# Optimization experiments

Hardware: AMD Instinct MI355X
Metric: run time of the kernel (lower is better)

## Reference

```python
import jax, jax.numpy as jnp
import numpy as np

N, C, F = 64, 128, 2048


def setup_inputs() -> dict:
    key = jax.random.key(0)
    kx, ka = jax.random.split(key)
    X = jax.random.normal(kx, (N, C, F), dtype=jnp.float32)
    # Glorot-uniform init for A [C, C, F]: fan_in = C*F, fan_out = C*F
    limit = np.sqrt(6.0 / (C * F + C * F)).astype(np.float32)
    A = jax.random.uniform(ka, (C, C, F), dtype=jnp.float32, minval=-limit, maxval=limit)
    return {"X": X, "A": A}


def reference(X, A):
    # scores: reduce feature dim F -> [N, C, M]
    c = jnp.einsum('ncf,cmf->ncm', X, A)
    W = jax.nn.softmax(c, axis=-1)  # attention over source channels M
    # combine: mix channels of X with attention weights -> [N, C, F]
    return jnp.einsum('nmf,ncm->ncf', X, W)
```

## Files before the change

### kernel.cpp

```cpp
#include <hip/hip_runtime.h>
#include <hip/hip_bf16.h>


typedef __attribute__((ext_vector_type(8))) short bf16x8;
typedef __attribute__((ext_vector_type(4))) float f32x4;

#define PART_ELEMS (64 * 128 * 128)
#define WOFF_BYTES (4ull * PART_ELEMS * 4ull)

static __device__ __forceinline__ unsigned f2bf_pk(float a, float b) {
    unsigned ua = __float_as_uint(a);
    unsigned ub = __float_as_uint(b);
    ua = (ua + 0x7FFFu + ((ua >> 16) & 1u)) >> 16;
    ub = (ub + 0x7FFFu + ((ub >> 16) & 1u)) >> 16;
    return ua | (ub << 16);
}

__global__ __launch_bounds__(256, 2) void k_scores(const float* __restrict__ X,
                                                   const float* __restrict__ A,
                                                   float* __restrict__ part) {
    __shared__ short Xt[64 * 72];
    __shared__ short At[128 * 72];

    const int bx = blockIdx.x;
    const int c  = bx >> 2;
    const int p  = bx & 3;
    const int t  = threadIdx.x;
    const int l  = t & 63;
    const int w  = t >> 6;
    const int wn = (w & 1) * 32;
    const int wm = (w >> 1) * 64;
    const int l15 = l & 15;
    const int lg  = l >> 4;

    f32x4 acc[2][4];
#pragma unroll
    for (int i = 0; i < 2; ++i)
#pragma unroll
        for (int j = 0; j < 4; ++j) acc[i][j] = (f32x4)0.0f;

    const int fq    = (t & 15) * 4;
    const int rbase = t >> 4;

    const float* Xg = X + ((size_t)rbase * 128 + c) * 2048 + p * 512 + fq;
    const float* Ag = A + ((size_t)c * 128 + rbase) * 2048 + p * 512 + fq;

    for (int kb = 0; kb < 8; ++kb) {
        const int f0 = kb * 64;
#pragma unroll
        for (int j = 0; j < 4; ++j) {
            float4 v = *(const float4*)(Xg + (size_t)j * (16 * 128 * 2048) + f0);
            *(uint2*)&Xt[(rbase + 16 * j) * 72 + fq] =
                make_uint2(f2bf_pk(v.x, v.y), f2bf_pk(v.z, v.w));
        }
#pragma unroll
        for (int j = 0; j < 8; ++j) {
            float4 v = *(const float4*)(Ag + (size_t)j * (16 * 2048) + f0);
            *(uint2*)&At[(rbase + 16 * j) * 72 + fq] =
                make_uint2(f2bf_pk(v.x, v.y), f2bf_pk(v.z, v.w));
        }
        __syncthreads();
#pragma unroll
        for (int ks = 0; ks < 2; ++ks) {
            const int ko = ks * 32 + lg * 8;
            bf16x8 a[2], b[4];
#pragma unroll
            for (int i = 0; i < 2; ++i)
                a[i] = *(const bf16x8*)&Xt[(wn + 16 * i + l15) * 72 + ko];
#pragma unroll
            for (int j = 0; j < 4; ++j)
                b[j] = *(const bf16x8*)&At[(wm + 16 * j + l15) * 72 + ko];
#pragma unroll
            for (int i = 0; i < 2; ++i)
#pragma unroll
                for (int j = 0; j < 4; ++j)
                    acc[i][j] = __builtin_amdgcn_mfma_f32_16x16x32_bf16(a[i], b[j], acc[i][j], 0, 0, 0);
        }
        __syncthreads();
    }

    float* outp = part + (size_t)p * PART_ELEMS;
#pragma unroll
    for (int i = 0; i < 2; ++i) {
        const int nb = wn + 16 * i + lg * 4;
#pragma unroll
        for (int j = 0; j < 4; ++j) {
            const int m = wm + 16 * j + l15;
#pragma unroll
            for (int r = 0; r < 4; ++r)
                outp[(size_t)(nb + r) * 16384 + c * 128 + m] = acc[i][j][r];
        }
    }
}

__global__ __launch_bounds__(256) void k_softmax(const float* __restrict__ part,
                                                 unsigned int* __restrict__ Wout) {
    const int t   = threadIdx.x;
    const int l   = t & 63;
    const int row = blockIdx.x * 4 + (t >> 6);

    const float* s = part + (size_t)row * 128 + 2 * l;
    float v0 = 0.f, v1 = 0.f;
#pragma unroll
    for (int p = 0; p < 4; ++p) {
        float2 v = *(const float2*)(s + (size_t)p * PART_ELEMS);
        v0 += v.x; v1 += v.y;
    }
    float mx = fmaxf(v0, v1);
#pragma unroll
    for (int d = 1; d < 64; d <<= 1) mx = fmaxf(mx, __shfl_xor(mx, d, 64));
    float e0 = __expf(v0 - mx), e1 = __expf(v1 - mx);
    float sm = e0 + e1;
#pragma unroll
    for (int d = 1; d < 64; d <<= 1) sm += __shfl_xor(sm, d, 64);
    const float inv = 1.0f / sm;
    Wout[(size_t)row * 64 + l] = f2bf_pk(e0 * inv, e1 * inv);
}

__global__ __launch_bounds__(256, 2) void k_combine(const float* __restrict__ X,
                                                    const unsigned short* __restrict__ W,
                                                    float* __restrict__ out) {
    __shared__ short Wl[128 * 136];
    __shared__ short T[128 * 40];

    const int bx = blockIdx.x;
    const int n  = bx >> 4;
    const int f0 = (bx & 15) * 128;
    const int t  = threadIdx.x;
    const int l  = t & 63;
    const int w  = t >> 6;
    const int l15 = l & 15;
    const int lg  = l >> 4;
    const int wc = (w >> 1) * 64;
    const int wf = (w & 1) * 64;

    {
        const int c = t >> 1;
        const int h = (t & 1) * 64;
        const unsigned short* src = W + ((size_t)n * 128 + c) * 128 + h;
#pragma unroll
        for (int j = 0; j < 8; ++j) {
            bf16x8 v = *(const bf16x8*)(src + j * 8);
            *(bf16x8*)&Wl[c * 136 + h + j * 8] = v;
        }
    }

    f32x4 acc[4][4];
#pragma unroll
    for (int i = 0; i < 4; ++i)
#pragma unroll
        for (int j = 0; j < 4; ++j) acc[i][j] = (f32x4)0.0f;

    const int mpr = (t & 15) * 2;
    const int fqu = (t >> 4) * 4;

    for (int m0 = 0; m0 < 128; m0 += 32) {
        __syncthreads();
#pragma unroll
        for (int pass = 0; pass < 2; ++pass) {
            const int fl = fqu + 64 * pass;
            const float* g = X + ((size_t)n * 128 + m0 + mpr) * 2048 + f0 + fl;
            float4 x0 = *(const float4*)g;
            float4 x1 = *(const float4*)(g + 2048);
            unsigned* Tw = (unsigned*)T;
            Tw[(fl + 0) * 20 + (mpr >> 1)] = f2bf_pk(x0.x, x1.x);
            Tw[(fl + 1) * 20 + (mpr >> 1)] = f2bf_pk(x0.y, x1.y);
            Tw[(fl + 2) * 20 + (mpr >> 1)] = f2bf_pk(x0.z, x1.z);
            Tw[(fl + 3) * 20 + (mpr >> 1)] = f2bf_pk(x0.w, x1.w);
        }
        __syncthreads();
        const int ko = lg * 8;
        bf16x8 a[4], b[4];
#pragma unroll
        for (int i = 0; i < 4; ++i)
            a[i] = *(const bf16x8*)&Wl[(wc + 16 * i + l15) * 136 + m0 + ko];
#pragma unroll
        for (int j = 0; j < 4; ++j)
            b[j] = *(const bf16x8*)&T[(wf + 16 * j + l15) * 40 + ko];
#pragma unroll
        for (int i = 0; i < 4; ++i)
#pragma unroll
            for (int j = 0; j < 4; ++j)
                acc[i][j] = __builtin_amdgcn_mfma_f32_16x16x32_bf16(a[i], b[j], acc[i][j], 0, 0, 0);
    }

#pragma unroll
    for (int i = 0; i < 4; ++i) {
        const int c = wc + 16 * i + lg * 4;
#pragma unroll
        for (int j = 0; j < 4; ++j) {
            const int f = f0 + wf + 16 * j + l15;
            float* o = out + ((size_t)n * 128 + c) * 2048 + f;
#pragma unroll
            for (int r = 0; r < 4; ++r) o[(size_t)r * 2048] = acc[i][j][r];
        }
    }
}

extern "C" void kernel_launch(void* const* d_in, const int* in_sizes, int n_in,
                              void* d_out, int out_size, void* d_ws, size_t ws_size,
                              hipStream_t stream) {
    const float* X = (const float*)d_in[0];
    const float* A = (const float*)d_in[1];
    float* out = (float*)d_out;

    float* part = (float*)d_ws;
    unsigned short* W = (unsigned short*)((char*)d_ws + WOFF_BYTES);

    k_scores<<<dim3(512), dim3(256), 0, stream>>>(X, A, part);
    k_softmax<<<dim3(2048), dim3(256), 0, stream>>>(part, (unsigned int*)W);
    k_combine<<<dim3(1024), dim3(256), 0, stream>>>(X, W, out);
}
```

Baseline: 283.1 us.

## Use direct global-to-LDS loads, bf16 partials, and 8-way F split

Both GEMM kernels now load fp32 tiles straight into LDS with global_load_lds using XOR-swizzled layouts, and convert to bf16 at fragment-read time instead of through registers before the LDS store. The score kernel splits F into 8 parts instead of 4, doubling block count, and raises the occupancy hint. Partial scores are stored as bf16, halving partial traffic to softmax. The bf16 partial sums lose precision before softmax, and storing fp32 in LDS doubles its footprint per tile.

```diff
diff --git a/kernel.cpp b/kernel.cpp
--- a/kernel.cpp
+++ b/kernel.cpp
@@ -1,12 +1,11 @@
 #include <hip/hip_runtime.h>
-#include <hip/hip_bf16.h>
 
 
 typedef __attribute__((ext_vector_type(8))) short bf16x8;
 typedef __attribute__((ext_vector_type(4))) float f32x4;
 
-#define PART_ELEMS (64 * 128 * 128)
-#define WOFF_BYTES (4ull * PART_ELEMS * 4ull)
+#define PART_E (64 * 128 * 128)
+#define NP 8
 
 static __device__ __forceinline__ unsigned f2bf_pk(float a, float b) {
     unsigned ua = __float_as_uint(a);
@@ -15,23 +14,46 @@
     ub = (ub + 0x7FFFu + ((ub >> 16) & 1u)) >> 16;
     return ua | (ub << 16);
 }
-
-__global__ __launch_bounds__(256, 2) void k_scores(const float* __restrict__ X,
+static __device__ __forceinline__ unsigned short f2bf1(float a) {
+    unsigned ua = __float_as_uint(a);
+    ua = (ua + 0x7FFFu + ((ua >> 16) & 1u)) >> 16;
+    return (unsigned short)ua;
+}
+static __device__ __forceinline__ float bf2f(unsigned s) {
+    return __uint_as_float(s << 16);
+}
+static __device__ __forceinline__ void gl_lds16(const void* g, void* l) {
+    __builtin_amdgcn_global_load_lds((const __attribute__((address_space(1))) void*)g,
+                                     (__attribute__((address_space(3))) void*)l, 16, 0, 0);
+}
+static __device__ __forceinline__ bf16x8 cvt8(float4 lo, float4 hi) {
+    union { bf16x8 v; unsigned u[4]; } r;
+    r.u[0] = f2bf_pk(lo.x, lo.y);
+    r.u[1] = f2bf_pk(lo.z, lo.w);
+    r.u[2] = f2bf_pk(hi.x, hi.y);
+    r.u[3] = f2bf_pk(hi.z, hi.w);
+    return r.v;
+}
+
+__global__ __launch_bounds__(256, 4) void k_scores(const float* __restrict__ X,
                                                    const float* __restrict__ A,
-                                                   float* __restrict__ part) {
-    __shared__ short Xt[64 * 72];
-    __shared__ short At[128 * 72];
+                                                   unsigned short* __restrict__ part) {
+    __shared__ float Xs[64 * 32];
+    __shared__ float As[128 * 32];
 
     const int bx = blockIdx.x;
-    const int c  = bx >> 2;
-    const int p  = bx & 3;
-    const int t  = threadIdx.x;
-    const int l  = t & 63;
-    const int w  = t >> 6;
+    const int c = bx >> 3;
+    const int p = bx & 7;
+    const int t = threadIdx.x;
+    const int l = t & 63;
+    const int w = t >> 6;
+    const int l15 = l & 15;
+    const int lg = l >> 4;
     const int wn = (w & 1) * 32;
     const int wm = (w >> 1) * 64;
-    const int l15 = l & 15;
-    const int lg  = l >> 4;
+
+    const int lr = l >> 3;
+    const int lq = (l & 7) ^ lr;
 
     f32x4 acc[2][4];
 #pragma unroll
@@ -39,47 +61,45 @@
 #pragma unroll
         for (int j = 0; j < 4; ++j) acc[i][j] = (f32x4)0.0f;
 
-    const int fq    = (t & 15) * 4;
-    const int rbase = t >> 4;
-
-    const float* Xg = X + ((size_t)rbase * 128 + c) * 2048 + p * 512 + fq;
-    const float* Ag = A + ((size_t)c * 128 + rbase) * 2048 + p * 512 + fq;
+    const int s0 = (lg * 2) ^ (l15 & 7);
+    const int s1 = (lg * 2 + 1) ^ (l15 & 7);
 
     for (int kb = 0; kb < 8; ++kb) {
-        const int f0 = kb * 64;
-#pragma unroll
-        for (int j = 0; j < 4; ++j) {
-            float4 v = *(const float4*)(Xg + (size_t)j * (16 * 128 * 2048) + f0);
-            *(uint2*)&Xt[(rbase + 16 * j) * 72 + fq] =
-                make_uint2(f2bf_pk(v.x, v.y), f2bf_pk(v.z, v.w));
-        }
-#pragma unroll
-        for (int j = 0; j < 8; ++j) {
-            float4 v = *(const float4*)(Ag + (size_t)j * (16 * 2048) + f0);
-            *(uint2*)&At[(rbase + 16 * j) * 72 + fq] =
-                make_uint2(f2bf_pk(v.x, v.y), f2bf_pk(v.z, v.w));
-        }
-        __syncthreads();
-#pragma unroll
-        for (int ks = 0; ks < 2; ++ks) {
-            const int ko = ks * 32 + lg * 8;
-            bf16x8 a[2], b[4];
-#pragma unroll
-            for (int i = 0; i < 2; ++i)
-                a[i] = *(const bf16x8*)&Xt[(wn + 16 * i + l15) * 72 + ko];
+        const int f = p * 256 + kb * 32 + lq * 4;
+#pragma unroll
+        for (int ii = 0; ii < 2; ++ii) {
+            const int I = 2 * w + ii;
+            const int r = I * 8 + lr;
+            gl_lds16(X + ((size_t)r * 128 + c) * 2048 + f, &Xs[I * 256]);
+        }
+#pragma unroll
+        for (int ii = 0; ii < 4; ++ii) {
+            const int I = 4 * w + ii;
+            const int r = I * 8 + lr;
+            gl_lds16(A + ((size_t)c * 128 + r) * 2048 + f, &As[I * 256]);
+        }
+        __syncthreads();
+
+        bf16x8 a[2], b[4];
+#pragma unroll
+        for (int i = 0; i < 2; ++i) {
+            const float4* row = (const float4*)&Xs[(wn + 16 * i + l15) * 32];
+            a[i] = cvt8(row[s0], row[s1]);
+        }
+#pragma unroll
+        for (int j = 0; j < 4; ++j) {
+            const float4* row = (const float4*)&As[(wm + 16 * j + l15) * 32];
+            b[j] = cvt8(row[s0], row[s1]);
+        }
+#pragma unroll
+        for (int i = 0; i < 2; ++i)
 #pragma unroll
             for (int j = 0; j < 4; ++j)
-                b[j] = *(const bf16x8*)&At[(wm + 16 * j + l15) * 72 + ko];
-#pragma unroll
-            for (int i = 0; i < 2; ++i)
-#pragma unroll
-                for (int j = 0; j < 4; ++j)
-                    acc[i][j] = __builtin_amdgcn_mfma_f32_16x16x32_bf16(a[i], b[j], acc[i][j], 0, 0, 0);
-        }
-        __syncthreads();
-    }
-
-    float* outp = part + (size_t)p * PART_ELEMS;
+                acc[i][j] = __builtin_amdgcn_mfma_f32_16x16x32_bf16(a[i], b[j], acc[i][j], 0, 0, 0);
+        __syncthreads();
+    }
+
+    unsigned short* op = part + (size_t)p * PART_E;
 #pragma unroll
     for (int i = 0; i < 2; ++i) {
         const int nb = wn + 16 * i + lg * 4;
@@ -88,23 +108,23 @@
             const int m = wm + 16 * j + l15;
 #pragma unroll
             for (int r = 0; r < 4; ++r)
-                outp[(size_t)(nb + r) * 16384 + c * 128 + m] = acc[i][j][r];
-        }
-    }
-}
-
-__global__ __launch_bounds__(256) void k_softmax(const float* __restrict__ part,
+                op[((size_t)(nb + r) * 128 + c) * 128 + m] = f2bf1(acc[i][j][r]);
+        }
+    }
+}
+
+__global__ __launch_bounds__(256) void k_softmax(const unsigned int* __restrict__ part,
                                                  unsigned int* __restrict__ Wout) {
-    const int t   = threadIdx.x;
-    const int l   = t & 63;
+    const int t = threadIdx.x;
+    const int l = t & 63;
     const int row = blockIdx.x * 4 + (t >> 6);
 
-    const float* s = part + (size_t)row * 128 + 2 * l;
     float v0 = 0.f, v1 = 0.f;
 #pragma unroll
-    for (int p = 0; p < 4; ++p) {
-        float2 v = *(const float2*)(s + (size_t)p * PART_ELEMS);
-        v0 += v.x; v1 += v.y;
+    for (int p = 0; p < NP; ++p) {
+        unsigned u = part[(size_t)p * (PART_E / 2) + (size_t)row * 64 + l];
+        v0 += bf2f(u & 0xFFFFu);
+        v1 += bf2f(u >> 16);
     }
     float mx = fmaxf(v0, v1);
 #pragma unroll
@@ -117,31 +137,32 @@
     Wout[(size_t)row * 64 + l] = f2bf_pk(e0 * inv, e1 * inv);
 }
 
-__global__ __launch_bounds__(256, 2) void k_combine(const float* __restrict__ X,
+__global__ __launch_bounds__(256, 3) void k_combine(const float* __restrict__ X,
                                                     const unsigned short* __restrict__ W,
                                                     float* __restrict__ out) {
-    __shared__ short Wl[128 * 136];
-    __shared__ short T[128 * 40];
+    __shared__ unsigned short Wl[128 * 128];
+    __shared__ float Xs[32 * 128];
 
     const int bx = blockIdx.x;
-    const int n  = bx >> 4;
+    const int n = bx >> 4;
     const int f0 = (bx & 15) * 128;
-    const int t  = threadIdx.x;
-    const int l  = t & 63;
-    const int w  = t >> 6;
+    const int t = threadIdx.x;
+    const int l = t & 63;
+    const int w = t >> 6;
     const int l15 = l & 15;
-    const int lg  = l >> 4;
+    const int lg = l >> 4;
     const int wc = (w >> 1) * 64;
     const int wf = (w & 1) * 64;
 
     {
-        const int c = t >> 1;
-        const int h = (t & 1) * 64;
-        const unsigned short* src = W + ((size_t)n * 128 + c) * 128 + h;
-#pragma unroll
-        for (int j = 0; j < 8; ++j) {
-            bf16x8 v = *(const bf16x8*)(src + j * 8);
-            *(bf16x8*)&Wl[c * 136 + h + j * 8] = v;
+        const int lr = l >> 4;
+        const int sl = l & 15;
+#pragma unroll
+        for (int ii = 0; ii < 8; ++ii) {
+            const int I = 8 * w + ii;
+            const int r = I * 4 + lr;
+            const int q = (sl & 8) | ((sl ^ r) & 7);
+            gl_lds16(W + (size_t)n * 16384 + r * 128 + q * 8, &Wl[I * 512]);
         }
     }
 
@@ -151,37 +172,45 @@
 #pragma unroll
         for (int j = 0; j < 4; ++j) acc[i][j] = (f32x4)0.0f;
 
-    const int mpr = (t & 15) * 2;
-    const int fqu = (t >> 4) * 4;
+    const int lr2 = l >> 5;
+    const int q2 = l & 31;
 
     for (int m0 = 0; m0 < 128; m0 += 32) {
-        __syncthreads();
-#pragma unroll
-        for (int pass = 0; pass < 2; ++pass) {
-            const int fl = fqu + 64 * pass;
-            const float* g = X + ((size_t)n * 128 + m0 + mpr) * 2048 + f0 + fl;
-            float4 x0 = *(const float4*)g;
-            float4 x1 = *(const float4*)(g + 2048);
-            unsigned* Tw = (unsigned*)T;
-            Tw[(fl + 0) * 20 + (mpr >> 1)] = f2bf_pk(x0.x, x1.x);
-            Tw[(fl + 1) * 20 + (mpr >> 1)] = f2bf_pk(x0.y, x1.y);
-            Tw[(fl + 2) * 20 + (mpr >> 1)] = f2bf_pk(x0.z, x1.z);
-            Tw[(fl + 3) * 20 + (mpr >> 1)] = f2bf_pk(x0.w, x1.w);
-        }
-        __syncthreads();
-        const int ko = lg * 8;
+#pragma unroll
+        for (int ii = 0; ii < 4; ++ii) {
+            const int I = 4 * w + ii;
+            const int r = I * 2 + lr2;
+            gl_lds16(X + ((size_t)n * 128 + m0 + r) * 2048 + f0 + q2 * 4, &Xs[I * 256]);
+        }
+        __syncthreads();
+
         bf16x8 a[4], b[4];
 #pragma unroll
-        for (int i = 0; i < 4; ++i)
-            a[i] = *(const bf16x8*)&Wl[(wc + 16 * i + l15) * 136 + m0 + ko];
-#pragma unroll
-        for (int j = 0; j < 4; ++j)
-            b[j] = *(const bf16x8*)&T[(wf + 16 * j + l15) * 40 + ko];
+        for (int i = 0; i < 4; ++i) {
+            const int cr = wc + 16 * i + l15;
+            const int q = (m0 >> 3) + lg;
+            const int s = (q & 8) | ((q ^ cr) & 7);
+            a[i] = *(const bf16x8*)&Wl[cr * 128 + s * 8];
+        }
+#pragma unroll
+        for (int j = 0; j < 4; ++j) {
+            const float* col = &Xs[(lg * 8) * 128 + wf + 16 * j + l15];
+            float v[8];
+#pragma unroll
+            for (int rr = 0; rr < 8; ++rr) v[rr] = col[rr * 128];
+            union { bf16x8 bv; unsigned u[4]; } r_;
+            r_.u[0] = f2bf_pk(v[0], v[1]);
+            r_.u[1] = f2bf_pk(v[2], v[3]);
+            r_.u[2] = f2bf_pk(v[4], v[5]);
+            r_.u[3] = f2bf_pk(v[6], v[7]);
+            b[j] = r_.bv;
+        }
 #pragma unroll
         for (int i = 0; i < 4; ++i)
 #pragma unroll
             for (int j = 0; j < 4; ++j)
                 acc[i][j] = __builtin_amdgcn_mfma_f32_16x16x32_bf16(a[i], b[j], acc[i][j], 0, 0, 0);
+        __syncthreads();
     }
 
 #pragma unroll
@@ -204,10 +233,10 @@
     const float* A = (const float*)d_in[1];
     float* out = (float*)d_out;
 
-    float* part = (float*)d_ws;
-    unsigned short* W = (unsigned short*)((char*)d_ws + WOFF_BYTES);
-
-    k_scores<<<dim3(512), dim3(256), 0, stream>>>(X, A, part);
-    k_softmax<<<dim3(2048), dim3(256), 0, stream>>>(part, (unsigned int*)W);
-    k_combine<<<dim3(1024), dim3(256), 0, stream>>>(X, W, out);
-}
+    unsigned short* part = (unsigned short*)d_ws;
+    unsigned short* Wb = part + (size_t)NP * PART_E;
+
+    k_scores<<<dim3(1024), dim3(256), 0, stream>>>(X, A, part);
+    k_softmax<<<dim3(2048), dim3(256), 0, stream>>>((const unsigned int*)part, (unsigned int*)Wb);
+    k_combine<<<dim3(1024), dim3(256), 0, stream>>>(X, Wb, out);
+}
```

Measured after the change: 286.6 us. About the same (+1.3%).
